# Kernel optimization log

Measured on AMD Instinct MI355X. Metric: run time of the kernel, lower is better.

Reference implementation:

```python
import jax, jax.numpy as jnp
import numpy as np

B, S, D, H = 4, 2048, 1024, 16
HD = D // H
FF = 4 * D
EPS = 1e-5


def setup_inputs() -> dict:
    key = jax.random.key(0)
    ks = jax.random.split(key, 12)
    s = lambda fan_in: 1.0 / np.sqrt(fan_in)
    inp = {
        "x": jax.random.normal(ks[0], (B, S, D), dtype=jnp.float32),
        # attention weights stored as (d_in, d_out)
        "Wq": jax.random.normal(ks[1], (D, D), dtype=jnp.float32) * s(D),
        "Wk": jax.random.normal(ks[2], (D, D), dtype=jnp.float32) * s(D),
        "Wv": jax.random.normal(ks[3], (D, D), dtype=jnp.float32) * s(D),
        "Wo": jax.random.normal(ks[4], (D, D), dtype=jnp.float32) * s(D),
        "bo": jnp.zeros((D,), dtype=jnp.float32),
        # feed-forward
        "W1": jax.random.normal(ks[5], (D, FF), dtype=jnp.float32) * s(D),
        "b1": jnp.zeros((FF,), dtype=jnp.float32),
        "W2": jax.random.normal(ks[6], (FF, D), dtype=jnp.float32) * s(FF),
        "b2": jnp.zeros((D,), dtype=jnp.float32),
        # layernorms
        "g1": jnp.ones((D,), dtype=jnp.float32),
        "be1": jnp.zeros((D,), dtype=jnp.float32),
        "g2": jnp.ones((D,), dtype=jnp.float32),
        "be2": jnp.zeros((D,), dtype=jnp.float32),
    }
    return inp


def _layernorm(x, gamma, beta):
    mean = jnp.mean(x, axis=-1, keepdims=True)
    var = jnp.mean(jnp.square(x - mean), axis=-1, keepdims=True)  # unbiased=False
    return gamma * (x - mean) / jnp.sqrt(var + EPS) + beta


def _gelu_tanh(x):
    c = jnp.sqrt(jnp.asarray(2.0 / jnp.pi, dtype=x.dtype))
    return 0.5 * x * (1.0 + jnp.tanh(c * (x + 0.044715 * x * x * x)))


def _block(x, Wq, Wk, Wv, Wo, bo, W1, b1, W2, b2, g1, be1, g2, be2):
    # --- pre-LN causal multi-head attention ---
    shortcut = x
    h = _layernorm(x, g1, be1)
    q = (h @ Wq).reshape(B, S, H, HD).transpose(0, 2, 1, 3)  # [B,H,S,HD]
    k = (h @ Wk).reshape(B, S, H, HD).transpose(0, 2, 1, 3)
    v = (h @ Wv).reshape(B, S, H, HD).transpose(0, 2, 1, 3)
    scores = jnp.einsum("bhqd,bhkd->bhqk", q, k)
    causal = jnp.tril(jnp.ones((S, S), dtype=bool))  # True = keep
    scores = jnp.where(causal, scores, -jnp.inf)
    attn = jax.nn.softmax(scores / jnp.sqrt(jnp.asarray(HD, scores.dtype)), axis=-1)
    ctx = jnp.einsum("bhqk,bhkd->bqhd", attn, v).reshape(B, S, D)
    x = ctx @ Wo + bo + shortcut
    # --- pre-LN GELU MLP ---
    shortcut = x
    h = _layernorm(x, g2, be2)
    h = _gelu_tanh(h @ W1 + b1) @ W2 + b2
    return h + shortcut


def reference(x, Wq, Wk, Wv, Wo, bo, W1, b1, W2, b2, g1, be1, g2, be2):
    return _block(x, Wq, Wk, Wv, Wo, bo, W1, b1, W2, b2, g1, be1, g2, be2)
```

## Files before the change

kernel.cpp:

```cpp
#include <hip/hip_runtime.h>
#include <cstdint>

#define B_   4
#define S_   2048
#define D_   1024
#define H_   16
#define HD_  64
#define FF_  4096
#define MTOK 8192

typedef short s16x8 __attribute__((ext_vector_type(8), may_alias));
typedef float f32x4 __attribute__((ext_vector_type(4)));
typedef unsigned short u16x4 __attribute__((ext_vector_type(4), may_alias));
typedef unsigned short u16x8 __attribute__((ext_vector_type(8), may_alias));

#define GLD_LDS16(g, l)                                                  \
  __builtin_amdgcn_global_load_lds(                                      \
      (__attribute__((address_space(1))) void*)(g),                      \
      (__attribute__((address_space(3))) void*)(l), 16, 0, 0)

__device__ __forceinline__ unsigned short f2bf(float f) {
  unsigned u = __float_as_uint(f);
  unsigned r = 0x7fffu + ((u >> 16) & 1u);
  return (unsigned short)((u + r) >> 16);
}

__global__ __launch_bounds__(256) void k_transpose(const float* __restrict__ in,
                                                   unsigned short* __restrict__ out,
                                                   int R, int C) {
  __shared__ float tile[32][33];
  int tx = threadIdx.x, ty = threadIdx.y;
  int c0 = blockIdx.x * 32, r0 = blockIdx.y * 32;
#pragma unroll
  for (int j = 0; j < 4; ++j)
    tile[ty + j * 8][tx] = in[(size_t)(r0 + ty + j * 8) * C + (c0 + tx)];
  __syncthreads();
#pragma unroll
  for (int j = 0; j < 4; ++j)
    out[(size_t)(c0 + ty + j * 8) * R + (r0 + tx)] = f2bf(tile[tx][ty + j * 8]);
}

__global__ __launch_bounds__(256) void k_layernorm(const float* __restrict__ x,
                                                   const float* __restrict__ g,
                                                   const float* __restrict__ be,
                                                   unsigned short* __restrict__ out) {
  int row = blockIdx.x, t = threadIdx.x;
  const float4* xr = (const float4*)(x + (size_t)row * D_);
  float4 v = xr[t];
  float s = v.x + v.y + v.z + v.w;
  float q = v.x * v.x + v.y * v.y + v.z * v.z + v.w * v.w;
#pragma unroll
  for (int o = 1; o < 64; o <<= 1) { s += __shfl_xor(s, o); q += __shfl_xor(q, o); }
  __shared__ float red[8];
  int wid = t >> 6;
  if ((t & 63) == 0) { red[wid * 2] = s; red[wid * 2 + 1] = q; }
  __syncthreads();
  s = red[0] + red[2] + red[4] + red[6];
  q = red[1] + red[3] + red[5] + red[7];
  float mean = s * (1.0f / D_);
  float rstd = rsqrtf(q * (1.0f / D_) - mean * mean + 1e-5f);
  float4 gv = ((const float4*)g)[t];
  float4 bv = ((const float4*)be)[t];
  u16x4 o4;
  o4[0] = f2bf(gv.x * (v.x - mean) * rstd + bv.x);
  o4[1] = f2bf(gv.y * (v.y - mean) * rstd + bv.y);
  o4[2] = f2bf(gv.z * (v.z - mean) * rstd + bv.z);
  o4[3] = f2bf(gv.w * (v.w - mean) * rstd + bv.w);
  *(u16x4*)(out + (size_t)row * D_ + t * 4) = o4;
}

template <int MODE>
__global__ __launch_bounds__(256) void k_gemm_bt(
    const unsigned short* __restrict__ A, const unsigned short* __restrict__ Bt,
    const float* __restrict__ bias, const float* __restrict__ resid,
    unsigned short* __restrict__ outb, float* __restrict__ outf,
    int M, int N, int K) {
  __shared__ __align__(16) unsigned short As[128 * 32];
  __shared__ __align__(16) unsigned short Bs[128 * 32];
  const int tid = threadIdx.x;
  const int wid = tid >> 6, lane = tid & 63;
  const int nwg = gridDim.x * gridDim.y;
  const int id = blockIdx.y * gridDim.x + blockIdx.x;
  const int swz = (id & 7) * (nwg >> 3) + (id >> 3);
  const int m0 = (swz / gridDim.x) * 128, n0 = (swz % gridDim.x) * 128;
  const int wr = wid >> 1, wc = wid & 1;
  const int l16 = lane & 15, lg = lane >> 4;
  f32x4 acc[4][4];
#pragma unroll
  for (int m = 0; m < 4; ++m)
#pragma unroll
    for (int n = 0; n < 4; ++n) acc[m][n] = 0.0f;

  const unsigned short* aSrc[2];
  const unsigned short* bSrc[2];
  char* aDst[2];
  char* bDst[2];
#pragma unroll
  for (int i = 0; i < 2; ++i) {
    int chunk = (i * 4 + wid) * 64 + lane;
    int row = chunk >> 2, col = (chunk & 3) * 8;
    aSrc[i] = A + (size_t)(m0 + row) * K + col;
    bSrc[i] = Bt + (size_t)(n0 + row) * K + col;
    aDst[i] = (char*)As + (size_t)(i * 4 + wid) * 1024;
    bDst[i] = (char*)Bs + (size_t)(i * 4 + wid) * 1024;
  }
  const unsigned short* aRd = As + ((wr * 64 + l16) * 32 + lg * 8);
  const unsigned short* bRd = Bs + ((wc * 64 + l16) * 32 + lg * 8);

  for (int kt = 0; kt < K; kt += 32) {
    __syncthreads();
#pragma unroll
    for (int i = 0; i < 2; ++i) {
      GLD_LDS16(aSrc[i] + kt, aDst[i]);
      GLD_LDS16(bSrc[i] + kt, bDst[i]);
    }
    __syncthreads();
    s16x8 af[4], bfr[4];
#pragma unroll
    for (int m = 0; m < 4; ++m) af[m] = *(const s16x8*)(aRd + m * 16 * 32);
#pragma unroll
    for (int n = 0; n < 4; ++n) bfr[n] = *(const s16x8*)(bRd + n * 16 * 32);
#pragma unroll
    for (int m = 0; m < 4; ++m)
#pragma unroll
      for (int n = 0; n < 4; ++n)
        acc[m][n] = __builtin_amdgcn_mfma_f32_16x16x32_bf16(af[m], bfr[n], acc[m][n], 0, 0, 0);
  }

  const int colb = n0 + wc * 64 + l16;
  const int rowb = m0 + wr * 64 + (lg << 2);

#define ROWMAJOR_FLUSH(DSTPTR, NSTRIDE, COLBASE, XFORM)                        \
  {                                                                            \
    _Pragma("unroll")                                                          \
    for (int p = 0; p < 2; ++p) {                                              \
      if (wr == p) {                                                           \
        _Pragma("unroll")                                                      \
        for (int n = 0; n < 4; ++n) {                                          \
          _Pragma("unroll")                                                    \
          for (int m = 0; m < 4; ++m) {                                        \
            _Pragma("unroll")                                                  \
            for (int r = 0; r < 4; ++r) {                                      \
              float xv = acc[m][n][r];                                         \
              XFORM;                                                           \
              Rs[(m * 16 + lg * 4 + r) * 136 + wc * 64 + n * 16 + l16] = f2bf(xv); \
            }                                                                  \
          }                                                                    \
        }                                                                      \
      }                                                                        \
      __syncthreads();                                                         \
      const int row_l = tid >> 2, seg = tid & 3;                               \
      _Pragma("unroll")                                                        \
      for (int j = 0; j < 4; ++j) {                                            \
        u16x8 vv = *(const u16x8*)(Rs + row_l * 136 + seg * 32 + j * 8);       \
        *(u16x8*)((DSTPTR) + (size_t)(m0 + p * 64 + row_l) * (NSTRIDE) +       \
                  (COLBASE) + seg * 32 + j * 8) = vv;                          \
      }                                                                        \
      if (p == 0) __syncthreads();                                             \
    }                                                                          \
  }

  if constexpr (MODE == 1) {
    __shared__ __align__(16) unsigned short Rs[64 * 136];
    ROWMAJOR_FLUSH(outb, N, n0, {
      xv += bias[n0 + wc * 64 + n * 16 + l16];
      float uu = 0.7978845608028654f * (xv + 0.044715f * xv * xv * xv);
      xv = xv * __builtin_amdgcn_rcpf(1.0f + __builtin_amdgcn_exp2f(uu * -2.885390081777927f));
    });
    return;
  }

  if constexpr (MODE == 3) {
    __shared__ __align__(16) unsigned short Rs[64 * 136];
    unsigned short* qout = outb;
    unsigned short* kout = outb + (size_t)MTOK * D_;
    unsigned short* vout = outb + 2 * (size_t)MTOK * D_;
    if (n0 < 1024) {
      ROWMAJOR_FLUSH(qout, D_, n0, { xv *= 0.125f; });
    } else if (n0 < 2048) {
      ROWMAJOR_FLUSH(kout, D_, n0 - 1024, {});
    } else {
      const int vbase = (m0 >> 11) * 1024 + (n0 - 2048);
      const int srow0 = m0 & 2047;
#pragma unroll
      for (int p = 0; p < 2; ++p) {
        if (wc == p) {
#pragma unroll
          for (int n = 0; n < 4; ++n)
#pragma unroll
            for (int m = 0; m < 4; ++m) {
              u16x4 pk;
#pragma unroll
              for (int r = 0; r < 4; ++r) pk[r] = f2bf(acc[m][n][r]);
              *(u16x4*)(Rs + (n * 16 + l16) * 136 + wr * 64 + m * 16 + lg * 4) = pk;
            }
        }
        __syncthreads();
        const int row_l = tid >> 2, seg = tid & 3;
#pragma unroll
        for (int j = 0; j < 4; ++j) {
          u16x8 vv = *(const u16x8*)(Rs + row_l * 136 + seg * 32 + j * 8);
          *(u16x8*)(vout + (size_t)(vbase + p * 64 + row_l) * S_ + srow0 + seg * 32 + j * 8) = vv;
        }
        if (p == 0) __syncthreads();
      }
    }
    return;
  }

  if constexpr (MODE == 2) {
#pragma unroll
    for (int n = 0; n < 4; ++n) {
      int col = colb + n * 16;
      float bv = bias[col];
#pragma unroll
      for (int m = 0; m < 4; ++m)
#pragma unroll
        for (int r = 0; r < 4; ++r) {
          int row = rowb + m * 16 + r;
          float val = acc[m][n][r] + bv + resid[(size_t)row * N + col];
          outf[(size_t)row * N + col] = val;
        }
    }
  }
#undef ROWMAJOR_FLUSH
}

__global__ __launch_bounds__(256, 3) void k_attn(
    const unsigned short* __restrict__ qg, const unsigned short* __restrict__ kg,
    const unsigned short* __restrict__ vtg, unsigned short* __restrict__ ctx) {
  const int id = blockIdx.x;
  const int bh = (id & 7) + 8 * (id >> 7);
  const int p  = (id >> 3) & 15;
  const int qtA = p, qtB = 31 - p;
  const int tid = threadIdx.x, wid = tid >> 6, lane = tid & 63;
  const int l16 = lane & 15, lg = lane >> 4;
  __shared__ __align__(16) unsigned short Ks[2][64 * 64];
  __shared__ __align__(16) unsigned short Vs[2][64 * 64];
  __shared__ __align__(16) unsigned short Ps[4][2][16 * 72];

  const size_t headoff = (size_t)(bh >> 4) * ((size_t)S_ * D_) + (size_t)(bh & 15) * HD_;
  const unsigned short* Kb = kg + headoff;
  const unsigned short* Vt = vtg + (size_t)bh * ((size_t)HD_ * S_);

  const int qrowA = qtA * 64 + wid * 16 + l16;
  const int qrowB = qtB * 64 + wid * 16 + l16;
  s16x8 qfA0 = *(const s16x8*)(qg + headoff + (size_t)qrowA * D_ + lg * 8);
  s16x8 qfA1 = *(const s16x8*)(qg + headoff + (size_t)qrowA * D_ + 32 + lg * 8);
  s16x8 qfB0 = *(const s16x8*)(qg + headoff + (size_t)qrowB * D_ + lg * 8);
  s16x8 qfB1 = *(const s16x8*)(qg + headoff + (size_t)qrowB * D_ + 32 + lg * 8);

  f32x4 oA[4], oB[4];
#pragma unroll
  for (int n = 0; n < 4; ++n) { oA[n] = (f32x4)0.0f; oB[n] = (f32x4)0.0f; }
  float lsumA[4] = {0.f, 0.f, 0.f, 0.f};
  float lsumB[4] = {0.f, 0.f, 0.f, 0.f};
  unsigned short* psA = &Ps[wid][0][0];
  unsigned short* psB = &Ps[wid][1][0];
  const int myrowA = qtA * 64 + wid * 16 + lg * 4;
  const int myrowB = qtB * 64 + wid * 16 + lg * 4;
  const float L2E = 1.4426950408889634f;

  const unsigned short* kSrc[2];
  const unsigned short* vSrc[2];
  int dstOff[2];
#pragma unroll
  for (int i = 0; i < 2; ++i) {
    int chunk = (i * 4 + wid) * 64 + lane;
    int row = chunk >> 3, pc = chunk & 7;
    int scol = (pc ^ (row & 7)) * 8;
    kSrc[i] = Kb + (size_t)row * D_ + scol;
    vSrc[i] = Vt + (size_t)row * S_ + scol;
    dstOff[i] = (i * 4 + wid) * 1024;
  }

#pragma unroll
  for (int i = 0; i < 2; ++i) {
    GLD_LDS16(kSrc[i], (char*)Ks[0] + dstOff[i]);
    GLD_LDS16(vSrc[i], (char*)Vs[0] + dstOff[i]);
  }
  __syncthreads();

  for (int t = 0; t <= qtB; ++t) {
    const int cur = t & 1;
    const int kv0 = t * 64;
    const bool doA = (t <= qtA);
    if (t < qtB) {
      const int kvn = kv0 + 64;
#pragma unroll
      for (int i = 0; i < 2; ++i) {
        GLD_LDS16(kSrc[i] + (size_t)kvn * D_, (char*)Ks[cur ^ 1] + dstOff[i]);
        GLD_LDS16(vSrc[i] + kvn, (char*)Vs[cur ^ 1] + dstOff[i]);
      }
    }
    const unsigned short* Kc = Ks[cur];
    const unsigned short* Vc = Vs[cur];
    s16x8 kf0[4], kf1[4];
#pragma unroll
    for (int n = 0; n < 4; ++n) {
      int srow = n * 16 + l16, sw = srow & 7;
      kf0[n] = *(const s16x8*)(Kc + srow * 64 + (lg ^ sw) * 8);
      kf1[n] = *(const s16x8*)(Kc + srow * 64 + ((4 + lg) ^ sw) * 8);
    }
    f32x4 saA[4], saB[4];
    if (doA) {
#pragma unroll
      for (int n = 0; n < 4; ++n) {
        saA[n] = (f32x4)0.0f;
        saA[n] = __builtin_amdgcn_mfma_f32_16x16x32_bf16(qfA0, kf0[n], saA[n], 0, 0, 0);
        saA[n] = __builtin_amdgcn_mfma_f32_16x16x32_bf16(qfA1, kf1[n], saA[n], 0, 0, 0);
      }
    }
#pragma unroll
    for (int n = 0; n < 4; ++n) {
      saB[n] = (f32x4)0.0f;
      saB[n] = __builtin_amdgcn_mfma_f32_16x16x32_bf16(qfB0, kf0[n], saB[n], 0, 0, 0);
      saB[n] = __builtin_amdgcn_mfma_f32_16x16x32_bf16(qfB1, kf1[n], saB[n], 0, 0, 0);
    }
    if (doA) {
      const bool mask = (t == qtA);
#pragma unroll
      for (int r = 0; r < 4; ++r)
#pragma unroll
        for (int n = 0; n < 4; ++n) {
          float pv = exp2f((saA[n][r] - 12.0f) * L2E);
          if (mask && (kv0 + n * 16 + l16) > (myrowA + r)) pv = 0.0f;
          lsumA[r] += pv;
          psA[(lg * 4 + r) * 72 + n * 16 + l16] = f2bf(pv);
        }
    }
    {
      const bool mask = (t == qtB);
#pragma unroll
      for (int r = 0; r < 4; ++r)
#pragma unroll
        for (int n = 0; n < 4; ++n) {
          float pv = exp2f((saB[n][r] - 12.0f) * L2E);
          if (mask && (kv0 + n * 16 + l16) > (myrowB + r)) pv = 0.0f;
          lsumB[r] += pv;
          psB[(lg * 4 + r) * 72 + n * 16 + l16] = f2bf(pv);
        }
    }
    s16x8 vf0[4], vf1[4];
#pragma unroll
    for (int n = 0; n < 4; ++n) {
      int srow = n * 16 + l16, sw = srow & 7;
      vf0[n] = *(const s16x8*)(Vc + srow * 64 + (lg ^ sw) * 8);
      vf1[n] = *(const s16x8*)(Vc + srow * 64 + ((4 + lg) ^ sw) * 8);
    }
    __builtin_amdgcn_sched_barrier(0);
    asm volatile("s_waitcnt lgkmcnt(0)" ::: "memory");
    __builtin_amdgcn_sched_barrier(0);
    {
      s16x8 paB0 = *(const s16x8*)(psB + l16 * 72 + lg * 8);
      s16x8 paB1 = *(const s16x8*)(psB + l16 * 72 + 32 + lg * 8);
#pragma unroll
      for (int n = 0; n < 4; ++n) {
        oB[n] = __builtin_amdgcn_mfma_f32_16x16x32_bf16(paB0, vf0[n], oB[n], 0, 0, 0);
        oB[n] = __builtin_amdgcn_mfma_f32_16x16x32_bf16(paB1, vf1[n], oB[n], 0, 0, 0);
      }
      if (doA) {
        s16x8 paA0 = *(const s16x8*)(psA + l16 * 72 + lg * 8);
        s16x8 paA1 = *(const s16x8*)(psA + l16 * 72 + 32 + lg * 8);
#pragma unroll
        for (int n = 0; n < 4; ++n) {
          oA[n] = __builtin_amdgcn_mfma_f32_16x16x32_bf16(paA0, vf0[n], oA[n], 0, 0, 0);
          oA[n] = __builtin_amdgcn_mfma_f32_16x16x32_bf16(paA1, vf1[n], oA[n], 0, 0, 0);
        }
      }
    }
    __syncthreads();
  }

#pragma unroll
  for (int r = 0; r < 4; ++r) {
    float la = lsumA[r], lb = lsumB[r];
    la += __shfl_xor(la, 1); lb += __shfl_xor(lb, 1);
    la += __shfl_xor(la, 2); lb += __shfl_xor(lb, 2);
    la += __shfl_xor(la, 4); lb += __shfl_xor(lb, 4);
    la += __shfl_xor(la, 8); lb += __shfl_xor(lb, 8);
    float ia = 1.0f / la, ib = 1.0f / lb;
#pragma unroll
    for (int n = 0; n < 4; ++n) {
      ctx[headoff + (size_t)(myrowA + r) * D_ + n * 16 + l16] = f2bf(oA[n][r] * ia);
      ctx[headoff + (size_t)(myrowB + r) * D_ + n * 16 + l16] = f2bf(oB[n][r] * ib);
    }
  }
}

extern "C" void kernel_launch(void* const* d_in, const int* in_sizes, int n_in,
                              void* d_out, int out_size, void* d_ws, size_t ws_size,
                              hipStream_t stream) {
  (void)in_sizes; (void)n_in; (void)out_size; (void)ws_size;
  const float* x   = (const float*)d_in[0];
  const float* Wq  = (const float*)d_in[1];
  const float* Wk  = (const float*)d_in[2];
  const float* Wv  = (const float*)d_in[3];
  const float* Wo  = (const float*)d_in[4];
  const float* bo  = (const float*)d_in[5];
  const float* W1  = (const float*)d_in[6];
  const float* b1  = (const float*)d_in[7];
  const float* W2  = (const float*)d_in[8];
  const float* b2  = (const float*)d_in[9];
  const float* g1  = (const float*)d_in[10];
  const float* be1 = (const float*)d_in[11];
  const float* g2  = (const float*)d_in[12];
  const float* be2 = (const float*)d_in[13];
  float* out = (float*)d_out;

  char* w = (char*)d_ws;
  const size_t MB = 1ull << 20;
  unsigned short* wqkvT = (unsigned short*)(w + 0 * MB);
  unsigned short* woT   = (unsigned short*)(w + 6 * MB);
  unsigned short* w1T   = (unsigned short*)(w + 8 * MB);
  unsigned short* w2T   = (unsigned short*)(w + 16 * MB);
  unsigned short* hb    = (unsigned short*)(w + 24 * MB);
  float*          x2    = (float*)(w + 40 * MB);
  unsigned short* qkv   = (unsigned short*)(w + 72 * MB);
  unsigned short* qb    = qkv;
  unsigned short* kb    = qkv + (size_t)MTOK * D_;
  unsigned short* vbT   = qkv + 2 * (size_t)MTOK * D_;
  unsigned short* cxb   = (unsigned short*)(w + 120 * MB);
  unsigned short* act   = (unsigned short*)(w + 72 * MB);

  dim3 tb(32, 8);
  k_transpose<<<dim3(32, 32), tb, 0, stream>>>(Wq, wqkvT, 1024, 1024);
  k_transpose<<<dim3(32, 32), tb, 0, stream>>>(Wk, wqkvT + 1024 * 1024, 1024, 1024);
  k_transpose<<<dim3(32, 32), tb, 0, stream>>>(Wv, wqkvT + 2048 * 1024, 1024, 1024);
  k_transpose<<<dim3(32, 32), tb, 0, stream>>>(Wo, woT, 1024, 1024);
  k_transpose<<<dim3(128, 32), tb, 0, stream>>>(W1, w1T, 1024, 4096);
  k_transpose<<<dim3(32, 128), tb, 0, stream>>>(W2, w2T, 4096, 1024);

  k_layernorm<<<MTOK, 256, 0, stream>>>(x, g1, be1, hb);

  k_gemm_bt<3><<<dim3(24, 64), 256, 0, stream>>>(hb, wqkvT, nullptr, nullptr, qkv, nullptr, MTOK, 3072, 1024);

  k_attn<<<1024, 256, 0, stream>>>(qb, kb, vbT, cxb);

  k_gemm_bt<2><<<dim3(8, 64), 256, 0, stream>>>(cxb, woT, bo, x, nullptr, x2, MTOK, 1024, 1024);

  k_layernorm<<<MTOK, 256, 0, stream>>>(x2, g2, be2, hb);

  k_gemm_bt<1><<<dim3(32, 64), 256, 0, stream>>>(hb, w1T, b1, nullptr, act, nullptr, MTOK, 4096, 1024);
  k_gemm_bt<2><<<dim3(8, 64), 256, 0, stream>>>(act, w2T, b2, x2, nullptr, out, MTOK, 1024, 4096);
}
```

Baseline: 475.4 us.

## Double-buffer GEMM LDS tiles to overlap global loads with MFMA compute

Splits the GEMM shared memory into two A and two B buffers. The main loop now issues the next K-tile's global-to-LDS loads before the MFMA work on the current tile, and needs one barrier per iteration instead of two. The epilogue staging buffer reuses the same shared allocation, so total LDS stays about the same. This is meant to hide global load latency behind matrix math, at the cost of slightly more address logic and relying on the barrier to wait for the async LDS loads.

Result: faster. 440.2 us (-7.4%).

```diff
diff --git a/kernel.cpp b/kernel.cpp
--- a/kernel.cpp
+++ b/kernel.cpp
@@ -75,8 +75,12 @@
     const float* __restrict__ bias, const float* __restrict__ resid,
     unsigned short* __restrict__ outb, float* __restrict__ outf,
     int M, int N, int K) {
-  __shared__ __align__(16) unsigned short As[128 * 32];
-  __shared__ __align__(16) unsigned short Bs[128 * 32];
+  __shared__ __align__(16) unsigned short smem[16384];
+  unsigned short* const As0 = smem;
+  unsigned short* const As1 = smem + 4096;
+  unsigned short* const Bs0 = smem + 8192;
+  unsigned short* const Bs1 = smem + 12288;
+  unsigned short* const Rs  = smem;
   const int tid = threadIdx.x;
   const int wid = tid >> 6, lane = tid & 63;
   const int nwg = gridDim.x * gridDim.y;
@@ -93,28 +97,39 @@
 
   const unsigned short* aSrc[2];
   const unsigned short* bSrc[2];
-  char* aDst[2];
-  char* bDst[2];
+  int dstOff[2];
 #pragma unroll
   for (int i = 0; i < 2; ++i) {
     int chunk = (i * 4 + wid) * 64 + lane;
     int row = chunk >> 2, col = (chunk & 3) * 8;
     aSrc[i] = A + (size_t)(m0 + row) * K + col;
     bSrc[i] = Bt + (size_t)(n0 + row) * K + col;
-    aDst[i] = (char*)As + (size_t)(i * 4 + wid) * 1024;
-    bDst[i] = (char*)Bs + (size_t)(i * 4 + wid) * 1024;
-  }
-  const unsigned short* aRd = As + ((wr * 64 + l16) * 32 + lg * 8);
-  const unsigned short* bRd = Bs + ((wc * 64 + l16) * 32 + lg * 8);
-
-  for (int kt = 0; kt < K; kt += 32) {
-    __syncthreads();
-#pragma unroll
-    for (int i = 0; i < 2; ++i) {
-      GLD_LDS16(aSrc[i] + kt, aDst[i]);
-      GLD_LDS16(bSrc[i] + kt, bDst[i]);
-    }
-    __syncthreads();
+    dstOff[i] = (i * 4 + wid) * 1024;
+  }
+  const int rdOffA = (wr * 64 + l16) * 32 + lg * 8;
+  const int rdOffB = (wc * 64 + l16) * 32 + lg * 8;
+
+#pragma unroll
+  for (int i = 0; i < 2; ++i) {
+    GLD_LDS16(aSrc[i], (char*)As0 + dstOff[i]);
+    GLD_LDS16(bSrc[i], (char*)Bs0 + dstOff[i]);
+  }
+  __syncthreads();
+
+  int idx = 0;
+  for (int kt = 0; kt < K; kt += 32, ++idx) {
+    const int cur = idx & 1;
+    if (kt + 32 < K) {
+      char* aN = (char*)(cur ? As0 : As1);
+      char* bN = (char*)(cur ? Bs0 : Bs1);
+#pragma unroll
+      for (int i = 0; i < 2; ++i) {
+        GLD_LDS16(aSrc[i] + kt + 32, aN + dstOff[i]);
+        GLD_LDS16(bSrc[i] + kt + 32, bN + dstOff[i]);
+      }
+    }
+    const unsigned short* aRd = (cur ? As1 : As0) + rdOffA;
+    const unsigned short* bRd = (cur ? Bs1 : Bs0) + rdOffB;
     s16x8 af[4], bfr[4];
 #pragma unroll
     for (int m = 0; m < 4; ++m) af[m] = *(const s16x8*)(aRd + m * 16 * 32);
@@ -125,6 +140,7 @@
 #pragma unroll
       for (int n = 0; n < 4; ++n)
         acc[m][n] = __builtin_amdgcn_mfma_f32_16x16x32_bf16(af[m], bfr[n], acc[m][n], 0, 0, 0);
+    __syncthreads();
   }
 
   const int colb = n0 + wc * 64 + l16;
@@ -161,7 +177,6 @@
   }
 
   if constexpr (MODE == 1) {
-    __shared__ __align__(16) unsigned short Rs[64 * 136];
     ROWMAJOR_FLUSH(outb, N, n0, {
       xv += bias[n0 + wc * 64 + n * 16 + l16];
       float uu = 0.7978845608028654f * (xv + 0.044715f * xv * xv * xv);
@@ -171,7 +186,6 @@
   }
 
   if constexpr (MODE == 3) {
-    __shared__ __align__(16) unsigned short Rs[64 * 136];
     unsigned short* qout = outb;
     unsigned short* kout = outb + (size_t)MTOK * D_;
     unsigned short* vout = outb + 2 * (size_t)MTOK * D_;
```

## Replace GEMM with 512-thread 256-wide tiles and 4-stage async LDS pipeline

Applied to the files above, without the earlier changes.

Rewrites the bf16 GEMM kernel to use 512 threads with 128x256 or 256x256 output tiles and a four-buffer global-to-LDS prefetch pipeline. Explicit vmcnt waits and a single barrier per k-step replace the old two-barrier synchronous loop. LDS chunk addresses get an XOR swizzle to avoid bank conflicts, and MFMA runs at raised priority. The epilogue flushes are adapted to the wider tiles. In exchange, the larger tiles leave fewer workgroups for the N=1024 GEMMs, and register and LDS pressure rises.

Result: faster. 433.1 us (-8.9%).

```diff
diff --git a/kernel.cpp b/kernel.cpp
--- a/kernel.cpp
+++ b/kernel.cpp
@@ -69,99 +69,159 @@
   *(u16x4*)(out + (size_t)row * D_ + t * 4) = o4;
 }
 
-template <int MODE>
-__global__ __launch_bounds__(256) void k_gemm_bt(
+template <int MODE, int BM>
+__global__ __launch_bounds__(512, 2) void k_gemm256(
     const unsigned short* __restrict__ A, const unsigned short* __restrict__ Bt,
     const float* __restrict__ bias, const float* __restrict__ resid,
     unsigned short* __restrict__ outb, float* __restrict__ outf,
     int M, int N, int K) {
-  __shared__ __align__(16) unsigned short As[128 * 32];
-  __shared__ __align__(16) unsigned short Bs[128 * 32];
+  constexpr int BN = 256, BK = 32;
+  constexpr int FM = BM / 32;
+  constexpr int NGA = BM / 128;
+  constexpr int NGB = 2;
+  constexpr int NG = NGA + NGB;
+  constexpr int AE = BM * BK;
+  constexpr int BE = BN * BK;
+  constexpr int BUF_E = AE + BE;
+  __shared__ __align__(16) unsigned short smem[4 * BUF_E];
+  unsigned short* const Rs = smem;
+
   const int tid = threadIdx.x;
   const int wid = tid >> 6, lane = tid & 63;
+  const int l16 = lane & 15, lg = lane >> 4;
+  const int wr = wid >> 2, wc = wid & 3;
   const int nwg = gridDim.x * gridDim.y;
   const int id = blockIdx.y * gridDim.x + blockIdx.x;
   const int swz = (id & 7) * (nwg >> 3) + (id >> 3);
-  const int m0 = (swz / gridDim.x) * 128, n0 = (swz % gridDim.x) * 128;
-  const int wr = wid >> 1, wc = wid & 1;
-  const int l16 = lane & 15, lg = lane >> 4;
-  f32x4 acc[4][4];
-#pragma unroll
-  for (int m = 0; m < 4; ++m)
-#pragma unroll
-    for (int n = 0; n < 4; ++n) acc[m][n] = 0.0f;
-
-  const unsigned short* aSrc[2];
-  const unsigned short* bSrc[2];
-  char* aDst[2];
-  char* bDst[2];
-#pragma unroll
-  for (int i = 0; i < 2; ++i) {
-    int chunk = (i * 4 + wid) * 64 + lane;
-    int row = chunk >> 2, col = (chunk & 3) * 8;
-    aSrc[i] = A + (size_t)(m0 + row) * K + col;
-    bSrc[i] = Bt + (size_t)(n0 + row) * K + col;
-    aDst[i] = (char*)As + (size_t)(i * 4 + wid) * 1024;
-    bDst[i] = (char*)Bs + (size_t)(i * 4 + wid) * 1024;
-  }
-  const unsigned short* aRd = As + ((wr * 64 + l16) * 32 + lg * 8);
-  const unsigned short* bRd = Bs + ((wc * 64 + l16) * 32 + lg * 8);
-
-  for (int kt = 0; kt < K; kt += 32) {
-    __syncthreads();
-#pragma unroll
-    for (int i = 0; i < 2; ++i) {
-      GLD_LDS16(aSrc[i] + kt, aDst[i]);
-      GLD_LDS16(bSrc[i] + kt, bDst[i]);
-    }
-    __syncthreads();
-    s16x8 af[4], bfr[4];
-#pragma unroll
-    for (int m = 0; m < 4; ++m) af[m] = *(const s16x8*)(aRd + m * 16 * 32);
-#pragma unroll
-    for (int n = 0; n < 4; ++n) bfr[n] = *(const s16x8*)(bRd + n * 16 * 32);
-#pragma unroll
-    for (int m = 0; m < 4; ++m)
+  const int m0 = (swz / gridDim.x) * BM, n0 = (swz % gridDim.x) * BN;
+
+  f32x4 acc[FM][4];
+#pragma unroll
+  for (int m = 0; m < FM; ++m)
+#pragma unroll
+    for (int n = 0; n < 4; ++n) acc[m][n] = (f32x4)0.0f;
+
+  const unsigned short* aSrc[NGA]; int aDstB[NGA];
+  const unsigned short* bSrc[NGB]; int bDstB[NGB];
+#pragma unroll
+  for (int g = 0; g < NGA; ++g) {
+    int q = g * 512 + tid, row = q >> 2, c = q & 3;
+    aSrc[g] = A + (size_t)(m0 + row) * K + (c ^ (row & 3)) * 8;
+    aDstB[g] = q * 16;
+  }
+#pragma unroll
+  for (int g = 0; g < NGB; ++g) {
+    int q = g * 512 + tid, row = q >> 2, c = q & 3;
+    bSrc[g] = Bt + (size_t)(n0 + row) * K + (c ^ (row & 3)) * 8;
+    bDstB[g] = q * 16;
+  }
+  const int sc = lg ^ (l16 & 3);
+  const int aOff = (wr * (BM / 2) + l16) * BK + sc * 8;
+  const int bOff = (wc * 64 + l16) * BK + sc * 8;
+
+#define STAGE(ti)                                                              \
+  {                                                                            \
+    const int _b = (ti) & 3;                                                   \
+    char* _pa = (char*)(smem + _b * BUF_E);                                    \
+    char* _pb = (char*)(smem + _b * BUF_E + AE);                               \
+    const int _kt = (ti) * BK;                                                 \
+    _Pragma("unroll")                                                          \
+    for (int g = 0; g < NGA; ++g) GLD_LDS16(aSrc[g] + _kt, _pa + aDstB[g]);    \
+    _Pragma("unroll")                                                          \
+    for (int g = 0; g < NGB; ++g) GLD_LDS16(bSrc[g] + _kt, _pb + bDstB[g]);    \
+  }
+
+  const int nt = K / BK;
+  STAGE(0); STAGE(1); STAGE(2);
+  if constexpr (NG == 4) { asm volatile("s_waitcnt vmcnt(8)" ::: "memory"); }
+  else                   { asm volatile("s_waitcnt vmcnt(6)" ::: "memory"); }
+  __builtin_amdgcn_sched_barrier(0);
+  __builtin_amdgcn_s_barrier();
+
+  for (int i = 0; i < nt; ++i) {
+    if (i + 3 < nt) STAGE(i + 3);
+    const unsigned short* pa = smem + (i & 3) * BUF_E + aOff;
+    const unsigned short* pb = smem + (i & 3) * BUF_E + AE + bOff;
+    s16x8 af[FM], bfr[4];
+#pragma unroll
+    for (int m = 0; m < FM; ++m) af[m] = *(const s16x8*)(pa + m * 16 * BK);
+#pragma unroll
+    for (int n = 0; n < 4; ++n) bfr[n] = *(const s16x8*)(pb + n * 16 * BK);
+    asm volatile("s_waitcnt lgkmcnt(0)" ::: "memory");
+    __builtin_amdgcn_sched_barrier(0);
+    __builtin_amdgcn_s_setprio(1);
+#pragma unroll
+    for (int m = 0; m < FM; ++m)
 #pragma unroll
       for (int n = 0; n < 4; ++n)
         acc[m][n] = __builtin_amdgcn_mfma_f32_16x16x32_bf16(af[m], bfr[n], acc[m][n], 0, 0, 0);
-  }
-
-  const int colb = n0 + wc * 64 + l16;
-  const int rowb = m0 + wr * 64 + (lg << 2);
+    __builtin_amdgcn_s_setprio(0);
+    if (i < nt - 3) {
+      if constexpr (NG == 4) { asm volatile("s_waitcnt vmcnt(8)" ::: "memory"); }
+      else                   { asm volatile("s_waitcnt vmcnt(6)" ::: "memory"); }
+    } else if (i == nt - 3) {
+      if constexpr (NG == 4) { asm volatile("s_waitcnt vmcnt(4)" ::: "memory"); }
+      else                   { asm volatile("s_waitcnt vmcnt(3)" ::: "memory"); }
+    } else if (i == nt - 2) {
+      asm volatile("s_waitcnt vmcnt(0)" ::: "memory");
+    }
+    __builtin_amdgcn_sched_barrier(0);
+    __builtin_amdgcn_s_barrier();
+  }
+#undef STAGE
+
+  if constexpr (MODE == 2) {
+#pragma unroll
+    for (int n = 0; n < 4; ++n) {
+      const int col = n0 + wc * 64 + n * 16 + l16;
+      const float bv = bias[col];
+#pragma unroll
+      for (int m = 0; m < FM; ++m)
+#pragma unroll
+        for (int r = 0; r < 4; ++r) {
+          const int row = m0 + wr * (BM / 2) + m * 16 + lg * 4 + r;
+          outf[(size_t)row * N + col] = acc[m][n][r] + bv + resid[(size_t)row * N + col];
+        }
+    }
+    return;
+  }
+
+  constexpr int PASSES = BM / 64;
+  constexpr int PPW = BM / 128;
 
 #define ROWMAJOR_FLUSH(DSTPTR, NSTRIDE, COLBASE, XFORM)                        \
   {                                                                            \
     _Pragma("unroll")                                                          \
-    for (int p = 0; p < 2; ++p) {                                              \
-      if (wr == p) {                                                           \
+    for (int p = 0; p < PASSES; ++p) {                                         \
+      if (wr == p / PPW) {                                                     \
+        const int mb = (p % PPW) * 4;                                          \
         _Pragma("unroll")                                                      \
         for (int n = 0; n < 4; ++n) {                                          \
           _Pragma("unroll")                                                    \
-          for (int m = 0; m < 4; ++m) {                                        \
+          for (int mm = 0; mm < 4; ++mm) {                                     \
             _Pragma("unroll")                                                  \
             for (int r = 0; r < 4; ++r) {                                      \
-              float xv = acc[m][n][r];                                         \
+              float xv = acc[mb + mm][n][r];                                   \
               XFORM;                                                           \
-              Rs[(m * 16 + lg * 4 + r) * 136 + wc * 64 + n * 16 + l16] = f2bf(xv); \
+              Rs[(mm * 16 + lg * 4 + r) * 264 + wc * 64 + n * 16 + l16] = f2bf(xv); \
             }                                                                  \
           }                                                                    \
         }                                                                      \
       }                                                                        \
       __syncthreads();                                                         \
-      const int row_l = tid >> 2, seg = tid & 3;                               \
+      const int row_l = tid >> 3;                                              \
       _Pragma("unroll")                                                        \
       for (int j = 0; j < 4; ++j) {                                            \
-        u16x8 vv = *(const u16x8*)(Rs + row_l * 136 + seg * 32 + j * 8);       \
+        const int c = (tid & 7) * 4 + j;                                       \
+        u16x8 vv = *(const u16x8*)(Rs + row_l * 264 + c * 8);                  \
         *(u16x8*)((DSTPTR) + (size_t)(m0 + p * 64 + row_l) * (NSTRIDE) +       \
-                  (COLBASE) + seg * 32 + j * 8) = vv;                          \
+                  (COLBASE) + c * 8) = vv;                                     \
       }                                                                        \
-      if (p == 0) __syncthreads();                                             \
+      if (p < PASSES - 1) __syncthreads();                                     \
     }                                                                          \
   }
 
   if constexpr (MODE == 1) {
-    __shared__ __align__(16) unsigned short Rs[64 * 136];
     ROWMAJOR_FLUSH(outb, N, n0, {
       xv += bias[n0 + wc * 64 + n * 16 + l16];
       float uu = 0.7978845608028654f * (xv + 0.044715f * xv * xv * xv);
@@ -171,7 +231,6 @@
   }
 
   if constexpr (MODE == 3) {
-    __shared__ __align__(16) unsigned short Rs[64 * 136];
     unsigned short* qout = outb;
     unsigned short* kout = outb + (size_t)MTOK * D_;
     unsigned short* vout = outb + 2 * (size_t)MTOK * D_;
@@ -182,46 +241,32 @@
     } else {
       const int vbase = (m0 >> 11) * 1024 + (n0 - 2048);
       const int srow0 = m0 & 2047;
-#pragma unroll
-      for (int p = 0; p < 2; ++p) {
-        if (wc == p) {
+      constexpr int CPT = BM / 64;
+#pragma unroll
+      for (int g = 0; g < 4; ++g) {
+        if (wc == g) {
 #pragma unroll
           for (int n = 0; n < 4; ++n)
 #pragma unroll
-            for (int m = 0; m < 4; ++m) {
+            for (int m = 0; m < FM; ++m) {
               u16x4 pk;
 #pragma unroll
               for (int r = 0; r < 4; ++r) pk[r] = f2bf(acc[m][n][r]);
-              *(u16x4*)(Rs + (n * 16 + l16) * 136 + wr * 64 + m * 16 + lg * 4) = pk;
+              *(u16x4*)(Rs + (n * 16 + l16) * 264 + wr * (BM / 2) + m * 16 + lg * 4) = pk;
             }
         }
         __syncthreads();
-        const int row_l = tid >> 2, seg = tid & 3;
-#pragma unroll
-        for (int j = 0; j < 4; ++j) {
-          u16x8 vv = *(const u16x8*)(Rs + row_l * 136 + seg * 32 + j * 8);
-          *(u16x8*)(vout + (size_t)(vbase + p * 64 + row_l) * S_ + srow0 + seg * 32 + j * 8) = vv;
-        }
-        if (p == 0) __syncthreads();
+        const int row_l = tid >> 3;
+#pragma unroll
+        for (int j = 0; j < CPT; ++j) {
+          const int c = (tid & 7) * CPT + j;
+          u16x8 vv = *(const u16x8*)(Rs + row_l * 264 + c * 8);
+          *(u16x8*)(vout + (size_t)(vbase + g * 64 + row_l) * S_ + srow0 + c * 8) = vv;
+        }
+        if (g < 3) __syncthreads();
       }
     }
     return;
-  }
-
-  if constexpr (MODE == 2) {
-#pragma unroll
-    for (int n = 0; n < 4; ++n) {
-      int col = colb + n * 16;
-      float bv = bias[col];
-#pragma unroll
-      for (int m = 0; m < 4; ++m)
-#pragma unroll
-        for (int r = 0; r < 4; ++r) {
-          int row = rowb + m * 16 + r;
-          float val = acc[m][n][r] + bv + resid[(size_t)row * N + col];
-          outf[(size_t)row * N + col] = val;
-        }
-    }
   }
 #undef ROWMAJOR_FLUSH
 }
@@ -433,14 +478,14 @@
 
   k_layernorm<<<MTOK, 256, 0, stream>>>(x, g1, be1, hb);
 
-  k_gemm_bt<3><<<dim3(24, 64), 256, 0, stream>>>(hb, wqkvT, nullptr, nullptr, qkv, nullptr, MTOK, 3072, 1024);
+  k_gemm256<3, 128><<<dim3(12, 64), 512, 0, stream>>>(hb, wqkvT, nullptr, nullptr, qkv, nullptr, MTOK, 3072, 1024);
 
   k_attn<<<1024, 256, 0, stream>>>(qb, kb, vbT, cxb);
 
-  k_gemm_bt<2><<<dim3(8, 64), 256, 0, stream>>>(cxb, woT, bo, x, nullptr, x2, MTOK, 1024, 1024);
+  k_gemm256<2, 128><<<dim3(4, 64), 512, 0, stream>>>(cxb, woT, bo, x, nullptr, x2, MTOK, 1024, 1024);
 
   k_layernorm<<<MTOK, 256, 0, stream>>>(x2, g2, be2, hb);
 
-  k_gemm_bt<1><<<dim3(32, 64), 256, 0, stream>>>(hb, w1T, b1, nullptr, act, nullptr, MTOK, 4096, 1024);
-  k_gemm_bt<2><<<dim3(8, 64), 256, 0, stream>>>(act, w2T, b2, x2, nullptr, out, MTOK, 1024, 4096);
-}
+  k_gemm256<1, 256><<<dim3(16, 32), 512, 0, stream>>>(hb, w1T, b1, nullptr, act, nullptr, MTOK, 4096, 1024);
+  k_gemm256<2, 128><<<dim3(4, 64), 512, 0, stream>>>(act, w2T, b2, x2, nullptr, out, MTOK, 1024, 4096);
+}
```
